# Performance work log

Hardware: AMD Instinct MI355X
Metric: run time of the kernel (lower is better)

Reference implementation:

```python
import jax, jax.numpy as jnp
import numpy as np

ETA, ALPHA, BETA, TAU, PROB_TH = 1.0, 0.08, 0.01, 10.0, 0.8


def knn_similarity(x, y, method):
    # x, y: [b, n, f]. Faithful port of GCN_Fusion.knn_similarity.
    b, n, f = x.shape
    if method == 'euclidean':
        # torch: D[b,i,j] = ||x[b,j] - y[b,i]||  (rows indexed by y)
        sq = (jnp.sum(y * y, -1)[:, :, None] + jnp.sum(x * x, -1)[:, None, :]
              - 2.0 * jnp.einsum('bif,bjf->bij', y, x))
        D = jnp.sqrt(jnp.maximum(sq, 1e-12))
    else:  # cosine: D[b,i,j] = 1 - <x_i, y_j>  (rows indexed by x)
        xn = x / jnp.maximum(jnp.linalg.norm(x, axis=2, keepdims=True), 1e-12)
        yn = y / jnp.maximum(jnp.linalg.norm(y, axis=2, keepdims=True), 1e-12)
        D = 1.0 - jnp.einsum('bif,bjf->bij', xn, yn)
    D_max = jnp.max(D, axis=2, keepdims=True)
    D_norm = D / D_max
    mu = jnp.mean(D, axis=(1, 2))
    sigma = jnp.std(D, axis=(1, 2), ddof=1)  # torch.std is unbiased
    prob_D = jax.nn.softmax(-D / TAU, axis=2)
    entropy = -jnp.sum(prob_D * jnp.log(prob_D + 1e-8), axis=2)  # [b,n]
    decay = jnp.exp(-ETA * entropy)[:, :, None]
    T = mu[:, None, None] + ALPHA * sigma[:, None, None] + BETA * (1.0 - D_norm) * decay
    sorted_idx = jnp.argsort(D, axis=-1)
    sorted_probs = jnp.take_along_axis(prob_D, sorted_idx, axis=-1)
    cum = jnp.cumsum(sorted_probs, axis=-1)
    mask = cum > PROB_TH
    first_over = jnp.argmax(mask.astype(jnp.int32), axis=-1)
    has_true = jnp.any(mask, axis=-1)
    num_edges = jnp.where(has_true, first_over, n)
    ranks = jnp.arange(n)
    mask_selected = ranks[None, None, :] < num_edges[:, :, None]
    # scatter_(-1, sorted_idx, mask_selected)  ==  gather by inverse permutation
    inv = jnp.argsort(sorted_idx, axis=-1)
    adj_mask = jnp.take_along_axis(mask_selected, inv, axis=-1)
    return (adj_mask & (D < T)).astype(D.dtype)


def gcn_fusion(x1, x2, x3, w1, b1, w2, b2, w3, b3):
    b, c, h, w = x1.shape
    n = h * w
    f1 = x1.reshape(b, c, n).transpose(0, 2, 1)  # [b,n,c]
    f2 = x2.reshape(b, c, n).transpose(0, 2, 1)
    f3 = x3.reshape(b, c, n).transpose(0, 2, 1)
    A11 = knn_similarity(f1, f1, 'euclidean')
    A22 = knn_similarity(f2, f2, 'euclidean')
    A33 = knn_similarity(f3, f3, 'euclidean')
    A12 = knn_similarity(f1, f2, 'cosine')
    A21 = knn_similarity(f2, f1, 'cosine')
    A13 = knn_similarity(f1, f3, 'cosine')
    A31 = knn_similarity(f3, f1, 'cosine')
    A23 = knn_similarity(f2, f3, 'cosine')
    A32 = knn_similarity(f3, f2, 'cosine')
    # 1x1 convs, expressed on flattened features: [b,n,c_out]
    p1 = jnp.einsum('bnc,oc->bno', f1, w1) + b1
    p2 = jnp.einsum('bnc,oc->bno', f2, w2) + b2
    p3 = jnp.einsum('bnc,oc->bno', f3, w3) + b3
    att = lambda a, pi, pj: jax.nn.softmax(a * jnp.einsum('bic,bjc->bij', pi, pj), axis=2)
    att_1 = jnp.concatenate([att(A11, p1, p1), att(A12, p1, p2), att(A13, p1, p3)], axis=2)
    att_2 = jnp.concatenate([att(A21, p2, p1), att(A22, p2, p2), att(A23, p2, p3)], axis=2)
    att_3 = jnp.concatenate([att(A31, p3, p1), att(A32, p3, p2), att(A33, p3, p3)], axis=2)
    x_cat = jnp.concatenate([f1, f2, f3], axis=1)  # [b,3n,c]
    o = (jnp.einsum('bij,bjc->bic', att_1, x_cat)
         + jnp.einsum('bij,bjc->bic', att_2, x_cat)
         + jnp.einsum('bij,bjc->bic', att_3, x_cat))
    return o.transpose(0, 2, 1).reshape(b, c, h, w)


def setup_inputs() -> dict:
    key = jax.random.key(0)
    ks = jax.random.split(key, 9)
    B, C, H, W = 2, 64, 32, 32
    s = 1.0 / np.sqrt(C)
    return {
        'x1': jax.random.normal(ks[0], (B, C, H, W), jnp.float32),
        'x2': jax.random.normal(ks[1], (B, C, H, W), jnp.float32),
        'x3': jax.random.normal(ks[2], (B, C, H, W), jnp.float32),
        'w1': jax.random.normal(ks[3], (C, C), jnp.float32) * s,
        'b1': jax.random.normal(ks[4], (C,), jnp.float32) * 0.01,
        'w2': jax.random.normal(ks[5], (C, C), jnp.float32) * s,
        'b2': jax.random.normal(ks[6], (C,), jnp.float32) * 0.01,
        'w3': jax.random.normal(ks[7], (C, C), jnp.float32) * s,
        'b3': jax.random.normal(ks[8], (C,), jnp.float32) * 0.01,
    }


def reference(x1, x2, x3, w1, b1, w2, b2, w3, b3):
    return gcn_fusion(x1, x2, x3, w1, b1, w2, b2, w3, b3)
```

## Files before the change

kernel.cpp:

```cpp
#include <hip/hip_runtime.h>

#define NN 1024
#define CC 64
#define BB 2

typedef unsigned long long ull;
typedef unsigned int u32;

#define WVB() __builtin_amdgcn_wave_barrier()

__device__ __forceinline__ float wsum(float v){
  #pragma unroll
  for (int o=32;o;o>>=1) v += __shfl_xor(v,o);
  return v;
}
__device__ __forceinline__ float wmaxr(float v){
  #pragma unroll
  for (int o=32;o;o>>=1) v = fmaxf(v, __shfl_xor(v,o));
  return v;
}
__device__ __forceinline__ float wminr(float v){
  #pragma unroll
  for (int o=32;o;o>>=1) v = fminf(v, __shfl_xor(v,o));
  return v;
}
__device__ __forceinline__ ull wmaxu64(ull v){
  #pragma unroll
  for (int o=32;o;o>>=1){ ull x = __shfl_xor(v,o); v = (x>v)?x:v; }
  return v;
}
__device__ __forceinline__ float4 ld4(const float* p){ return *reinterpret_cast<const float4*>(p); }
__device__ __forceinline__ u32 monob(float d){
  u32 u = __float_as_uint(d);
  return (u & 0x80000000u) ? ~u : (u | 0x80000000u);
}

#define GEMM_COLS(R, col, ylm, j4v, adv)                                          \
  { _Pragma("unroll 4")                                                           \
    for (int cc=0; cc<16; cc++){                                                  \
      float4 c0 = ld4((col) + (size_t)(cc*4+0)*NN + (j4v));                       \
      float4 c1 = ld4((col) + (size_t)(cc*4+1)*NN + (j4v));                       \
      float4 c2 = ld4((col) + (size_t)(cc*4+2)*NN + (j4v));                       \
      float4 c3 = ld4((col) + (size_t)(cc*4+3)*NN + (j4v));                       \
      _Pragma("unroll")                                                           \
      for (int rr=0; rr<(R); rr++){                                               \
        float4 y4 = *reinterpret_cast<const float4*>(&(ylm)[rr][cc*4]);           \
        float a0 = adv[rr][0], a1 = adv[rr][1], a2 = adv[rr][2], a3 = adv[rr][3]; \
        a0 = fmaf(y4.x,c0.x,a0); a0 = fmaf(y4.y,c1.x,a0); a0 = fmaf(y4.z,c2.x,a0); a0 = fmaf(y4.w,c3.x,a0); \
        a1 = fmaf(y4.x,c0.y,a1); a1 = fmaf(y4.y,c1.y,a1); a1 = fmaf(y4.z,c2.y,a1); a1 = fmaf(y4.w,c3.y,a1); \
        a2 = fmaf(y4.x,c0.z,a2); a2 = fmaf(y4.y,c1.z,a2); a2 = fmaf(y4.z,c2.z,a2); a2 = fmaf(y4.w,c3.z,a2); \
        a3 = fmaf(y4.x,c0.w,a3); a3 = fmaf(y4.y,c1.w,a3); a3 = fmaf(y4.z,c2.w,a3); a3 = fmaf(y4.w,c3.w,a3); \
        adv[rr][0]=a0; adv[rr][1]=a1; adv[rr][2]=a2; adv[rr][3]=a3;               \
      }                                                                           \
    }                                                                             \
  }

#define DFINISH(eucv, yn2r, cn2v, adr, dvv)                                       \
  { if (eucv){                                                                    \
      dvv[0] = sqrtf(fmaxf(fmaf(-2.0f, adr[0], (yn2r) + (cn2v).x), 1e-12f));      \
      dvv[1] = sqrtf(fmaxf(fmaf(-2.0f, adr[1], (yn2r) + (cn2v).y), 1e-12f));      \
      dvv[2] = sqrtf(fmaxf(fmaf(-2.0f, adr[2], (yn2r) + (cn2v).z), 1e-12f));      \
      dvv[3] = sqrtf(fmaxf(fmaf(-2.0f, adr[3], (yn2r) + (cn2v).w), 1e-12f));      \
    } else {                                                                      \
      dvv[0] = 1.0f - adr[0]; dvv[1] = 1.0f - adr[1];                             \
      dvv[2] = 1.0f - adr[2]; dvv[3] = 1.0f - adr[3];                             \
    }                                                                             \
  }

__global__ void kz(float* __restrict__ out, double* __restrict__ sums){
  int i = blockIdx.x*256 + threadIdx.x;
  if (i < BB*CC*NN) out[i] = 0.0f;
  if (i < 36) sums[i] = 0.0;
}

__global__ __launch_bounds__(256)
void k0a(const float* __restrict__ x1, const float* __restrict__ x2, const float* __restrict__ x3,
         float* __restrict__ f){
  int bid = blockIdx.x;
  int tile = bid & 15;
  int b = (bid >> 4) & 1;
  int s = bid >> 5;
  const float* x = (s==0)?x1:((s==1)?x2:x3);
  __shared__ float lds[64][65];
  int i0 = tile*64;
  for (int idx = threadIdx.x; idx < 4096; idx += 256){
    int c = idx >> 6, ii = idx & 63;
    lds[c][ii] = x[(size_t)(b*CC + c)*NN + i0 + ii];
  }
  __syncthreads();
  for (int idx = threadIdx.x; idx < 4096; idx += 256){
    int ii = idx >> 6, c = idx & 63;
    f[((size_t)(s*BB + b)*NN + i0 + ii)*CC + c] = lds[c][ii];
  }
}

__global__ __launch_bounds__(256)
void k0b(const float* __restrict__ f,
         const float* __restrict__ w1, const float* __restrict__ b1,
         const float* __restrict__ w2, const float* __restrict__ b2,
         const float* __restrict__ w3, const float* __restrict__ b3,
         float* __restrict__ p, float* __restrict__ pT,
         float* __restrict__ fnT, float* __restrict__ nrm2g){
  int bid = blockIdx.x;
  int chunk = bid & 63;
  int b = (bid >> 6) & 1;
  int s = bid >> 7;
  const float* w = (s==0)?w1:((s==1)?w2:w3);
  const float* bias = (s==0)?b1:((s==1)?b2:b3);
  __shared__ float wl[64][65];
  __shared__ float fr[16][65];
  __shared__ float n2[16];
  int i0 = chunk*16;
  int t = threadIdx.x;
  for (int idx = t; idx < 4096; idx += 256){
    int o = idx >> 6, c = idx & 63;
    wl[o][c] = w[idx];
  }
  for (int idx = t; idx < 1024; idx += 256){
    int rr = idx >> 6, c = idx & 63;
    fr[rr][c] = f[((size_t)(s*BB + b)*NN + i0 + rr)*CC + c];
  }
  __syncthreads();
  {
    int r = t >> 4, l = t & 15;
    float pv = 0.f;
    for (int c = l; c < 64; c += 16) pv += fr[r][c]*fr[r][c];
    #pragma unroll
    for (int o=8;o;o>>=1) pv += __shfl_down(pv, o, 16);
    if (l == 0) n2[r] = pv;
  }
  __syncthreads();
  if (t < 16) nrm2g[(size_t)(s*BB + b)*NN + i0 + t] = n2[t];
  for (int idx = t; idx < 1024; idx += 256){
    int rr = idx >> 6, c = idx & 63;
    float rinv = 1.0f / fmaxf(sqrtf(n2[rr]), 1e-12f);
    fnT[((size_t)(s*BB + b)*CC + c)*NN + i0 + rr] = fr[rr][c]*rinv;
  }
  for (int idx = t; idx < 1024; idx += 256){
    int rr = idx >> 6, o = idx & 63;
    float acc = bias[o];
    #pragma unroll
    for (int c = 0; c < 64; c++) acc += fr[rr][c]*wl[o][c];
    p [((size_t)(s*BB + b)*NN + i0 + rr)*CC + o] = acc;
    pT[((size_t)(s*BB + b)*CC + o)*NN + i0 + rr] = acc;
  }
}

__global__ void k2(const double* __restrict__ sums, float* __restrict__ baseg){
  int t = threadIdx.x;
  if (t < 18){
    double S = sums[t*2], S2 = sums[t*2+1];
    const double Nsq = 1048576.0;
    double mu = S / Nsq;
    double var = (S2 - S*S/Nsq) / (Nsq - 1.0);
    double sg = var > 0.0 ? sqrt(var) : 0.0;
    baseg[t] = (float)(mu + 0.08*sg);
  }
}

__global__ __launch_bounds__(256, 3)
void ksel(const float* __restrict__ x1, const float* __restrict__ x2, const float* __restrict__ x3,
          const float* __restrict__ f, const float* __restrict__ fnT,
          const float* __restrict__ nrm2g, double* __restrict__ sums, uint4* __restrict__ rec){
  __shared__ __align__(16) float yl[8][64];
  __shared__ __align__(16) float Dt[8][NN];
  __shared__ float hist[4][256];
  __shared__ float candd[4][64];
  __shared__ int   candj[4][64];
  __shared__ u32   candb[4][64];
  __shared__ float yn2[8];
  __shared__ int   cnt4[4];
  __shared__ int   selI4[4];
  __shared__ float selC4[4];
  __shared__ float s1s[4], s2s[4];

  int bid = blockIdx.x;
  int tile = bid & 127;
  int q = (bid >> 7) % 9;
  int b = bid / 1152;
  int r = q / 3, s = q - 3*r;
  bool euc = (r == s);
  int m = b*9 + q;
  int i0 = tile*8;
  int t = threadIdx.x;
  int w = t >> 6, lane = t & 63;

  if (t < 8) yn2[t] = nrm2g[(size_t)(r*BB + b)*NN + i0 + t];
  __syncthreads();
  for (int idx = t; idx < 512; idx += 256){
    int rr = idx >> 6, c = idx & 63;
    float v = f[((size_t)(r*BB + b)*NN + i0 + rr)*CC + c];
    if (!euc) v *= 1.0f / fmaxf(sqrtf(yn2[rr]), 1e-12f);
    yl[rr][c] = v;
  }
  __syncthreads();

  const float* xs = (s==0)?x1:((s==1)?x2:x3);
  const float* colD = euc ? (xs + (size_t)(b*CC)*NN) : (fnT + (size_t)((s*BB + b)*CC)*NN);
  int j4 = 4*t;

  float ad[8][4];
  #pragma unroll
  for (int rr=0;rr<8;rr++){ ad[rr][0]=0.f; ad[rr][1]=0.f; ad[rr][2]=0.f; ad[rr][3]=0.f; }
  GEMM_COLS(8, colD, yl, j4, ad)

  float4 cn2 = make_float4(0.f,0.f,0.f,0.f);
  if (euc) cn2 = ld4(nrm2g + (size_t)(s*BB + b)*NN + j4);

  float sd = 0.f, sd2 = 0.f;
  #pragma unroll
  for (int rr=0;rr<8;rr++){
    float dv[4];
    DFINISH(euc, yn2[rr], cn2, ad[rr], dv)
    sd  += dv[0]+dv[1]+dv[2]+dv[3];
    sd2 += dv[0]*dv[0]+dv[1]*dv[1]+dv[2]*dv[2]+dv[3]*dv[3];
    float4 o4; o4.x=dv[0]; o4.y=dv[1]; o4.z=dv[2]; o4.w=dv[3];
    *reinterpret_cast<float4*>(&Dt[rr][j4]) = o4;
  }
  sd = wsum(sd); sd2 = wsum(sd2);
  if (lane == 0){ s1s[w] = sd; s2s[w] = sd2; }
  __syncthreads();
  if (t == 0){
    double S  = (double)s1s[0] + (double)s1s[1] + (double)s1s[2] + (double)s1s[3];
    double S2 = (double)s2s[0] + (double)s2s[1] + (double)s2s[2] + (double)s2s[3];
    atomicAdd(&sums[m*2 + 0], S);
    atomicAdd(&sums[m*2 + 1], S2);
  }

  for (int rr2 = 0; rr2 < 2; rr2++){
    int row = w*2 + rr2;
    float dreg[16];
    #pragma unroll
    for (int k2=0;k2<4;k2++){
      float4 v = ld4(&Dt[row][4*lane + 256*k2]);
      dreg[4*k2+0]=v.x; dreg[4*k2+1]=v.y; dreg[4*k2+2]=v.z; dreg[4*k2+3]=v.w;
    }
    float lmin = 3.4e38f, lmax = -3.4e38f;
    #pragma unroll
    for (int k=0;k<16;k++){ lmin = fminf(lmin,dreg[k]); lmax = fmaxf(lmax,dreg[k]); }
    float Dmin = wminr(lmin);
    float Dmax = wmaxr(lmax);
    float lz = 0.f;
    #pragma unroll
    for (int k=0;k<16;k++) lz += expf((Dmin - dreg[k])*0.1f);
    float Z = wsum(lz);
    float invZ = 1.0f/Z;
    float preg[16];
    #pragma unroll
    for (int k=0;k<16;k++) preg[k] = expf((Dmin - dreg[k])*0.1f)*invZ;
    float le = 0.f;
    #pragma unroll
    for (int k=0;k<16;k++) le += preg[k]*logf(preg[k] + 1e-8f);
    float ent = -wsum(le);
    float decay = expf(-ent);
    float range = Dmax - Dmin;
    float scale1 = 256.0f / fmaxf(range, 1e-30f);

    if (lane==0){ selI4[w]=255; selC4[w]=0.8f; cnt4[w]=0; }
    #pragma unroll
    for (int i=0;i<4;i++) hist[w][lane*4+i] = 0.f;
    WVB();
    #pragma unroll
    for (int k=0;k<16;k++){
      int b1 = (int)((dreg[k]-Dmin)*scale1); b1 = (b1>255)?255:b1;
      atomicAdd(&hist[w][b1], preg[k]);
    }
    WVB();
    {
      float h0=hist[w][lane*4+0], h1=hist[w][lane*4+1], h2=hist[w][lane*4+2], h3=hist[w][lane*4+3];
      float tot = h0+h1+h2+h3;
      float incl = tot;
      #pragma unroll
      for (int o=1;o<64;o<<=1){ float v = __shfl_up(incl,o); if (lane>=o) incl += v; }
      float excl = incl - tot;
      float c0=excl, c1=excl+h0, c2=c1+h1, c3=c2+h2;
      bool f0=(c0<=0.8f && 0.8f<c0+h0), f1=(c1<=0.8f && 0.8f<c1+h1),
           f2=(c2<=0.8f && 0.8f<c2+h2), f3=(c3<=0.8f && 0.8f<c3+h3);
      if (f0){ selI4[w]=lane*4+0; selC4[w]=c0; }
      if (f1){ selI4[w]=lane*4+1; selC4[w]=c1; }
      if (f2){ selI4[w]=lane*4+2; selC4[w]=c2; }
      if (f3){ selI4[w]=lane*4+3; selC4[w]=c3; }
      if (__ballot(f0||f1||f2||f3) == 0ull){
        int bi = 10000; float bc = 0.f;
        if (c0>0.8f){bi=lane*4+0;bc=c0;} else if (c1>0.8f){bi=lane*4+1;bc=c1;}
        else if (c2>0.8f){bi=lane*4+2;bc=c2;} else if (c3>0.8f){bi=lane*4+3;bc=c3;}
        int mn = bi;
        #pragma unroll
        for (int o=32;o;o>>=1) mn = min(mn, __shfl_xor(mn,o));
        if (mn==bi && bi<10000){ selI4[w]=bi; selC4[w]=bc; }
      }
    }
    WVB();
    int B1 = selI4[w]; float cb1 = selC4[w];
    float lo2 = Dmin + (float)B1/scale1;
    float scale2 = scale1*256.0f;
    if (lane==0){ selI4[w]=255; selC4[w]=cb1; }
    #pragma unroll
    for (int i=0;i<4;i++) hist[w][lane*4+i] = 0.f;
    WVB();
    #pragma unroll
    for (int k=0;k<16;k++){
      int b1 = (int)((dreg[k]-Dmin)*scale1); b1 = (b1>255)?255:b1;
      if (b1 == B1){
        int b2 = (int)((dreg[k]-lo2)*scale2); b2 = (b2<0)?0:((b2>255)?255:b2);
        atomicAdd(&hist[w][b2], preg[k]);
      }
    }
    WVB();
    {
      float h0=hist[w][lane*4+0], h1=hist[w][lane*4+1], h2=hist[w][lane*4+2], h3=hist[w][lane*4+3];
      float tot = h0+h1+h2+h3;
      float incl = tot;
      #pragma unroll
      for (int o=1;o<64;o<<=1){ float v = __shfl_up(incl,o); if (lane>=o) incl += v; }
      float excl = incl - tot;
      float c0=cb1+excl, c1=c0+h0, c2=c1+h1, c3=c2+h2;
      bool f0=(c0<=0.8f && 0.8f<c0+h0), f1=(c1<=0.8f && 0.8f<c1+h1),
           f2=(c2<=0.8f && 0.8f<c2+h2), f3=(c3<=0.8f && 0.8f<c3+h3);
      if (f0){ selI4[w]=lane*4+0; selC4[w]=c0; }
      if (f1){ selI4[w]=lane*4+1; selC4[w]=c1; }
      if (f2){ selI4[w]=lane*4+2; selC4[w]=c2; }
      if (f3){ selI4[w]=lane*4+3; selC4[w]=c3; }
      if (__ballot(f0||f1||f2||f3) == 0ull){
        int bi = 10000; float bc = 0.f;
        if (c0>0.8f){bi=lane*4+0;bc=c0;} else if (c1>0.8f){bi=lane*4+1;bc=c1;}
        else if (c2>0.8f){bi=lane*4+2;bc=c2;} else if (c3>0.8f){bi=lane*4+3;bc=c3;}
        int mn = bi;
        #pragma unroll
        for (int o=32;o;o>>=1) mn = min(mn, __shfl_xor(mn,o));
        if (mn==bi && bi<10000){ selI4[w]=bi; selC4[w]=bc; }
      }
    }
    WVB();
    int B2 = selI4[w]; float cb2 = selC4[w];

    #pragma unroll
    for (int k=0;k<16;k++){
      int b1 = (int)((dreg[k]-Dmin)*scale1); b1 = (b1>255)?255:b1;
      if (b1 == B1){
        int b2 = (int)((dreg[k]-lo2)*scale2); b2 = (b2<0)?0:((b2>255)?255:b2);
        if (b2 == B2){
          int c = atomicAdd(&cnt4[w], 1);
          if (c < 64){
            int j = (k>>2)*256 + 4*lane + (k&3);
            candj[w][c] = j;
            candd[w][c] = dreg[k];
            candb[w][c] = monob(dreg[k]);
          }
        }
      }
    }
    WVB();
    ull em = 0;
    #pragma unroll
    for (int k=0;k<16;k++){
      int b1 = (int)((dreg[k]-Dmin)*scale1); b1 = (b1>255)?255:b1;
      bool qual;
      if (b1 < B1) qual = true;
      else if (b1 > B1) qual = false;
      else {
        int b2 = (int)((dreg[k]-lo2)*scale2); b2 = (b2<0)?0:((b2>255)?255:b2);
        qual = (b2 < B2);
      }
      if (qual){
        int j = (k>>2)*256 + 4*lane + (k&3);
        ull key = ((ull)monob(dreg[k]) << 32) | (u32)j;
        if (key > em) em = key;
      }
    }
    em = wmaxu64(em);
    if (lane == 0){
      int n = cnt4[w]; n = (n>64)?64:n;
      ull best = em;
      for (int a=0;a<n;a++){
        float da = candd[w][a]; int ja = candj[w][a];
        float acc = cb2;
        for (int bb=0;bb<n;bb++){
          float db = candd[w][bb]; int jb = candj[w][bb];
          if (db < da || (db == da && jb <= ja))
            acc += expf((Dmin - db)*0.1f)*invZ;
        }
        if (acc <= 0.8f){
          ull key = ((ull)candb[w][a] << 32) | (u32)ja;
          if (key > best) best = key;
        }
      }
      rec[(size_t)m*NN + i0 + row] = make_uint4((u32)(best>>32), (u32)(best & 0xFFFFFFFFu),
                                               __float_as_uint(Dmax), __float_as_uint(decay));
    }
    WVB();
  }
}

__global__ __launch_bounds__(256, 3)
void kapp(const float* __restrict__ x1, const float* __restrict__ x2, const float* __restrict__ x3,
          const float* __restrict__ f, const float* __restrict__ p,
          const float* __restrict__ fnT, const float* __restrict__ pT,
          const float* __restrict__ nrm2g, const float* __restrict__ baseg,
          const uint4* __restrict__ rec, float* __restrict__ out){
  __shared__ __align__(16) float yl[8][64];
  __shared__ __align__(16) float pyl[8][64];
  __shared__ __align__(16) float Sm[8][NN];
  __shared__ __align__(16) float opart[4][8][64];
  __shared__ float yn2[8];
  __shared__ u32 dBb[8]; __shared__ u32 jBl[8];
  __shared__ float th[8];

  int bid = blockIdx.x;
  int tile = bid & 127;
  int q = (bid >> 7) % 9;
  int b = bid / 1152;
  int r = q / 3, s = q - 3*r;
  bool euc = (r == s);
  int m = b*9 + q;
  int i0 = tile*8;
  int t = threadIdx.x;
  int w = t >> 6, lane = t & 63;

  if (t < 8){
    yn2[t] = nrm2g[(size_t)(r*BB + b)*NN + i0 + t];
    uint4 R = rec[(size_t)m*NN + i0 + t];
    dBb[t] = R.x; jBl[t] = R.y;
    float Dmax = __uint_as_float(R.z);
    float decay = __uint_as_float(R.w);
    float Tb = baseg[m];
    th[t] = (Tb + 0.01f*decay) / (1.0f + 0.01f*decay/Dmax);
  }
  __syncthreads();
  for (int idx = t; idx < 512; idx += 256){
    int rr = idx >> 6, c = idx & 63;
    float v = f[((size_t)(r*BB + b)*NN + i0 + rr)*CC + c];
    if (!euc) v *= 1.0f / fmaxf(sqrtf(yn2[rr]), 1e-12f);
    yl[rr][c] = v;
    pyl[rr][c] = p[((size_t)(r*BB + b)*NN + i0 + rr)*CC + c];
  }
  __syncthreads();

  const float* xs = (s==0)?x1:((s==1)?x2:x3);
  const float* colD = euc ? (xs + (size_t)(b*CC)*NN) : (fnT + (size_t)((s*BB + b)*CC)*NN);
  const float* colP = pT + (size_t)((s*BB + b)*CC)*NN;
  int j4 = 4*t;

  float ad[8][4];
  #pragma unroll
  for (int rr=0;rr<8;rr++){ ad[rr][0]=0.f; ad[rr][1]=0.f; ad[rr][2]=0.f; ad[rr][3]=0.f; }
  GEMM_COLS(8, colD, yl, j4, ad)

  float ap[8][4];
  #pragma unroll
  for (int rr=0;rr<8;rr++){ ap[rr][0]=0.f; ap[rr][1]=0.f; ap[rr][2]=0.f; ap[rr][3]=0.f; }
  GEMM_COLS(8, colP, pyl, j4, ap)

  float4 cn2 = make_float4(0.f,0.f,0.f,0.f);
  if (euc) cn2 = ld4(nrm2g + (size_t)(s*BB + b)*NN + j4);

  #pragma unroll
  for (int rr=0;rr<8;rr++){
    float dv[4];
    DFINISH(euc, yn2[rr], cn2, ad[rr], dv)
    u32 db = dBb[rr]; u32 jb = jBl[rr]; float tt = th[rr];
    float4 sv;
    {
      u32 bits = monob(dv[0]); u32 j = (u32)(j4+0);
      bool sel = (bits < db) || (bits == db && j <= jb);
      sv.x = (sel && dv[0] < tt) ? ap[rr][0] : 0.f;
    }
    {
      u32 bits = monob(dv[1]); u32 j = (u32)(j4+1);
      bool sel = (bits < db) || (bits == db && j <= jb);
      sv.y = (sel && dv[1] < tt) ? ap[rr][1] : 0.f;
    }
    {
      u32 bits = monob(dv[2]); u32 j = (u32)(j4+2);
      bool sel = (bits < db) || (bits == db && j <= jb);
      sv.z = (sel && dv[2] < tt) ? ap[rr][2] : 0.f;
    }
    {
      u32 bits = monob(dv[3]); u32 j = (u32)(j4+3);
      bool sel = (bits < db) || (bits == db && j <= jb);
      sv.w = (sel && dv[3] < tt) ? ap[rr][3] : 0.f;
    }
    *reinterpret_cast<float4*>(&Sm[rr][j4]) = sv;
  }
  __syncthreads();

  #pragma unroll
  for (int e=0;e<2;e++){
    int row = 2*w + e;
    float s16[16];
    #pragma unroll
    for (int k2=0;k2<4;k2++){
      float4 v = ld4(&Sm[row][4*lane + 256*k2]);
      s16[4*k2+0]=v.x; s16[4*k2+1]=v.y; s16[4*k2+2]=v.z; s16[4*k2+3]=v.w;
    }
    float lm = -3.4e38f;
    #pragma unroll
    for (int k=0;k<16;k++) lm = fmaxf(lm, s16[k]);
    float M = wmaxr(lm);
    float ls = 0.f;
    #pragma unroll
    for (int k=0;k<16;k++) ls += expf(s16[k]-M);
    float Z2 = wsum(ls);
    float iZ2 = 1.0f/Z2;
    #pragma unroll
    for (int k2=0;k2<4;k2++){
      float4 v;
      v.x = expf(s16[4*k2+0]-M)*iZ2;
      v.y = expf(s16[4*k2+1]-M)*iZ2;
      v.z = expf(s16[4*k2+2]-M)*iZ2;
      v.w = expf(s16[4*k2+3]-M)*iZ2;
      *reinterpret_cast<float4*>(&Sm[row][4*lane + 256*k2]) = v;
    }
  }
  __syncthreads();

  int cg = t & 15, jj = t >> 4;
  float acc[8][4];
  #pragma unroll
  for (int rr=0;rr<8;rr++){ acc[rr][0]=0.f; acc[rr][1]=0.f; acc[rr][2]=0.f; acc[rr][3]=0.f; }
  const float* fs = f + (size_t)((s*BB + b)*NN)*CC;
  for (int mm=0; mm<64; mm++){
    int j = jj + 16*mm;
    float4 fv = ld4(&fs[(size_t)j*CC + 4*cg]);
    #pragma unroll
    for (int rr=0;rr<8;rr++){
      float pv = Sm[rr][j];
      acc[rr][0] = fmaf(pv, fv.x, acc[rr][0]);
      acc[rr][1] = fmaf(pv, fv.y, acc[rr][1]);
      acc[rr][2] = fmaf(pv, fv.z, acc[rr][2]);
      acc[rr][3] = fmaf(pv, fv.w, acc[rr][3]);
    }
  }
  #pragma unroll
  for (int rr=0;rr<8;rr++){
    #pragma unroll
    for (int i=0;i<4;i++){
      acc[rr][i] += __shfl_xor(acc[rr][i], 16);
      acc[rr][i] += __shfl_xor(acc[rr][i], 32);
    }
  }
  if (lane < 16){
    #pragma unroll
    for (int rr=0;rr<8;rr++){
      float4 v; v.x=acc[rr][0]; v.y=acc[rr][1]; v.z=acc[rr][2]; v.w=acc[rr][3];
      *reinterpret_cast<float4*>(&opart[w][rr][4*cg]) = v;
    }
  }
  __syncthreads();
  #pragma unroll
  for (int e=0;e<2;e++){
    int idx = t + 256*e;
    int rr = idx >> 6, c = idx & 63;
    float v = opart[0][rr][c]+opart[1][rr][c]+opart[2][rr][c]+opart[3][rr][c];
    atomicAdd(&out[(size_t)(b*CC + c)*NN + i0 + rr], v);
  }
}

extern "C" void kernel_launch(void* const* d_in, const int* in_sizes, int n_in,
                              void* d_out, int out_size, void* d_ws, size_t ws_size,
                              hipStream_t stream){
  const float* x1 = (const float*)d_in[0];
  const float* x2 = (const float*)d_in[1];
  const float* x3 = (const float*)d_in[2];
  const float* w1 = (const float*)d_in[3];
  const float* b1 = (const float*)d_in[4];
  const float* w2 = (const float*)d_in[5];
  const float* b2 = (const float*)d_in[6];
  const float* w3 = (const float*)d_in[7];
  const float* b3 = (const float*)d_in[8];

  char* ws = (char*)d_ws;
  const size_t SZ = (size_t)3*BB*NN*CC*sizeof(float);
  float*  f    = (float*)(ws);
  float*  p    = (float*)(ws + SZ);
  float*  fnT  = (float*)(ws + 2*SZ);
  float*  pT   = (float*)(ws + 3*SZ);
  float*  nrm2 = (float*)(ws + 4*SZ);
  double* sums = (double*)(ws + 4*SZ + 32768);
  float*  baseg= (float*)(ws + 4*SZ + 32768 + 512);
  uint4*  rec  = (uint4*)(ws + 4*SZ + 65536);

  float* out = (float*)d_out;

  kz  <<<512, 256, 0, stream>>>(out, sums);
  k0a <<<96,  256, 0, stream>>>(x1, x2, x3, f);
  k0b <<<384, 256, 0, stream>>>(f, w1, b1, w2, b2, w3, b3, p, pT, fnT, nrm2);
  ksel<<<2304,256, 0, stream>>>(x1, x2, x3, f, fnT, nrm2, sums, rec);
  k2  <<<1,   64,  0, stream>>>(sums, baseg);
  kapp<<<2304,256, 0, stream>>>(x1, x2, x3, f, p, fnT, pT, nrm2, baseg, rec, out);
}
```

Measured before the change: 389.5 us.

## Reuse softmax exps, closed-form entropy, skip second histogram, parallelize candidate scan

In the selection kernel the softmax exponentials are now computed once and reused. The entropy is rewritten algebraically as exp(sum p*logit)/Z, which avoids a per-element log. The second-level histogram pass now runs only when the first-level bucket holds more than 64 elements. The O(n^2) single-lane candidate cumulative-probability scan becomes a wave-parallel scan using stored probabilities. The attention softmax in kapp also reuses its exp results instead of recomputing them. The closed-form entropy drops the 1e-8 epsilon inside the log, so results differ slightly from the reference, and the cutoff comparison now orders candidates by monotone bits instead of the float distance values.

```diff
diff --git a/kernel.cpp b/kernel.cpp
--- a/kernel.cpp
+++ b/kernel.cpp
@@ -66,6 +66,8 @@
       dvv[2] = 1.0f - adr[2]; dvv[3] = 1.0f - adr[3];                             \
     }                                                                             \
   }
+
+#define BUCKET1(dv) ({ int _b = (int)(((dv)-Dmin)*scale1); (_b>255)?255:_b; })
 
 __global__ void kz(float* __restrict__ out, double* __restrict__ sums){
   int i = blockIdx.x*256 + threadIdx.x;
@@ -165,7 +167,7 @@
   __shared__ __align__(16) float yl[8][64];
   __shared__ __align__(16) float Dt[8][NN];
   __shared__ float hist[4][256];
-  __shared__ float candd[4][64];
+  __shared__ float candp[4][64];
   __shared__ int   candj[4][64];
   __shared__ u32   candb[4][64];
   __shared__ float yn2[8];
@@ -240,29 +242,29 @@
     for (int k=0;k<16;k++){ lmin = fminf(lmin,dreg[k]); lmax = fmaxf(lmax,dreg[k]); }
     float Dmin = wminr(lmin);
     float Dmax = wmaxr(lmax);
+    float preg[16];
     float lz = 0.f;
     #pragma unroll
-    for (int k=0;k<16;k++) lz += expf((Dmin - dreg[k])*0.1f);
+    for (int k=0;k<16;k++){ preg[k] = expf((Dmin - dreg[k])*0.1f); lz += preg[k]; }
     float Z = wsum(lz);
     float invZ = 1.0f/Z;
-    float preg[16];
-    #pragma unroll
-    for (int k=0;k<16;k++) preg[k] = expf((Dmin - dreg[k])*0.1f)*invZ;
-    float le = 0.f;
-    #pragma unroll
-    for (int k=0;k<16;k++) le += preg[k]*logf(preg[k] + 1e-8f);
-    float ent = -wsum(le);
-    float decay = expf(-ent);
+    #pragma unroll
+    for (int k=0;k<16;k++) preg[k] *= invZ;
+    float sl = 0.f;
+    #pragma unroll
+    for (int k=0;k<16;k++) sl = fmaf(preg[k], (Dmin - dreg[k])*0.1f, sl);
+    float sumpl = wsum(sl);
+    float decay = expf(sumpl)*invZ;
     float range = Dmax - Dmin;
     float scale1 = 256.0f / fmaxf(range, 1e-30f);
 
-    if (lane==0){ selI4[w]=255; selC4[w]=0.8f; cnt4[w]=0; }
+    if (lane==0){ selI4[w]=255; selC4[w]=0.8f; }
     #pragma unroll
     for (int i=0;i<4;i++) hist[w][lane*4+i] = 0.f;
     WVB();
     #pragma unroll
     for (int k=0;k<16;k++){
-      int b1 = (int)((dreg[k]-Dmin)*scale1); b1 = (b1>255)?255:b1;
+      int b1 = BUCKET1(dreg[k]);
       atomicAdd(&hist[w][b1], preg[k]);
     }
     WVB();
@@ -292,73 +294,93 @@
     }
     WVB();
     int B1 = selI4[w]; float cb1 = selC4[w];
-    float lo2 = Dmin + (float)B1/scale1;
-    float scale2 = scale1*256.0f;
-    if (lane==0){ selI4[w]=255; selC4[w]=cb1; }
-    #pragma unroll
-    for (int i=0;i<4;i++) hist[w][lane*4+i] = 0.f;
-    WVB();
-    #pragma unroll
-    for (int k=0;k<16;k++){
-      int b1 = (int)((dreg[k]-Dmin)*scale1); b1 = (b1>255)?255:b1;
-      if (b1 == B1){
-        int b2 = (int)((dreg[k]-lo2)*scale2); b2 = (b2<0)?0:((b2>255)?255:b2);
-        atomicAdd(&hist[w][b2], preg[k]);
-      }
-    }
-    WVB();
-    {
-      float h0=hist[w][lane*4+0], h1=hist[w][lane*4+1], h2=hist[w][lane*4+2], h3=hist[w][lane*4+3];
-      float tot = h0+h1+h2+h3;
-      float incl = tot;
+
+    float cntf = 0.f;
+    #pragma unroll
+    for (int k=0;k<16;k++) if (BUCKET1(dreg[k]) == B1) cntf += 1.0f;
+    float n1f = wsum(cntf);
+    bool need2 = (n1f > 64.0f);
+    float cb = cb1;
+    int B2 = 0; float lo2 = 0.f, scale2 = 0.f;
+    if (need2){
+      lo2 = Dmin + (float)B1/scale1;
+      scale2 = scale1*256.0f;
+      if (lane==0){ selI4[w]=255; selC4[w]=cb1; }
       #pragma unroll
-      for (int o=1;o<64;o<<=1){ float v = __shfl_up(incl,o); if (lane>=o) incl += v; }
-      float excl = incl - tot;
-      float c0=cb1+excl, c1=c0+h0, c2=c1+h1, c3=c2+h2;
-      bool f0=(c0<=0.8f && 0.8f<c0+h0), f1=(c1<=0.8f && 0.8f<c1+h1),
-           f2=(c2<=0.8f && 0.8f<c2+h2), f3=(c3<=0.8f && 0.8f<c3+h3);
-      if (f0){ selI4[w]=lane*4+0; selC4[w]=c0; }
-      if (f1){ selI4[w]=lane*4+1; selC4[w]=c1; }
-      if (f2){ selI4[w]=lane*4+2; selC4[w]=c2; }
-      if (f3){ selI4[w]=lane*4+3; selC4[w]=c3; }
-      if (__ballot(f0||f1||f2||f3) == 0ull){
-        int bi = 10000; float bc = 0.f;
-        if (c0>0.8f){bi=lane*4+0;bc=c0;} else if (c1>0.8f){bi=lane*4+1;bc=c1;}
-        else if (c2>0.8f){bi=lane*4+2;bc=c2;} else if (c3>0.8f){bi=lane*4+3;bc=c3;}
-        int mn = bi;
-        #pragma unroll
-        for (int o=32;o;o>>=1) mn = min(mn, __shfl_xor(mn,o));
-        if (mn==bi && bi<10000){ selI4[w]=bi; selC4[w]=bc; }
-      }
-    }
-    WVB();
-    int B2 = selI4[w]; float cb2 = selC4[w];
-
-    #pragma unroll
-    for (int k=0;k<16;k++){
-      int b1 = (int)((dreg[k]-Dmin)*scale1); b1 = (b1>255)?255:b1;
-      if (b1 == B1){
-        int b2 = (int)((dreg[k]-lo2)*scale2); b2 = (b2<0)?0:((b2>255)?255:b2);
-        if (b2 == B2){
-          int c = atomicAdd(&cnt4[w], 1);
-          if (c < 64){
-            int j = (k>>2)*256 + 4*lane + (k&3);
-            candj[w][c] = j;
-            candd[w][c] = dreg[k];
-            candb[w][c] = monob(dreg[k]);
-          }
+      for (int i=0;i<4;i++) hist[w][lane*4+i] = 0.f;
+      WVB();
+      #pragma unroll
+      for (int k=0;k<16;k++){
+        if (BUCKET1(dreg[k]) == B1){
+          int b2 = (int)((dreg[k]-lo2)*scale2); b2 = (b2<0)?0:((b2>255)?255:b2);
+          atomicAdd(&hist[w][b2], preg[k]);
         }
       }
-    }
+      WVB();
+      {
+        float h0=hist[w][lane*4+0], h1=hist[w][lane*4+1], h2=hist[w][lane*4+2], h3=hist[w][lane*4+3];
+        float tot = h0+h1+h2+h3;
+        float incl = tot;
+        #pragma unroll
+        for (int o=1;o<64;o<<=1){ float v = __shfl_up(incl,o); if (lane>=o) incl += v; }
+        float excl = incl - tot;
+        float c0=cb1+excl, c1=c0+h0, c2=c1+h1, c3=c2+h2;
+        bool f0=(c0<=0.8f && 0.8f<c0+h0), f1=(c1<=0.8f && 0.8f<c1+h1),
+             f2=(c2<=0.8f && 0.8f<c2+h2), f3=(c3<=0.8f && 0.8f<c3+h3);
+        if (f0){ selI4[w]=lane*4+0; selC4[w]=c0; }
+        if (f1){ selI4[w]=lane*4+1; selC4[w]=c1; }
+        if (f2){ selI4[w]=lane*4+2; selC4[w]=c2; }
+        if (f3){ selI4[w]=lane*4+3; selC4[w]=c3; }
+        if (__ballot(f0||f1||f2||f3) == 0ull){
+          int bi = 10000; float bc = 0.f;
+          if (c0>0.8f){bi=lane*4+0;bc=c0;} else if (c1>0.8f){bi=lane*4+1;bc=c1;}
+          else if (c2>0.8f){bi=lane*4+2;bc=c2;} else if (c3>0.8f){bi=lane*4+3;bc=c3;}
+          int mn = bi;
+          #pragma unroll
+          for (int o=32;o;o>>=1) mn = min(mn, __shfl_xor(mn,o));
+          if (mn==bi && bi<10000){ selI4[w]=bi; selC4[w]=bc; }
+        }
+      }
+      WVB();
+      B2 = selI4[w]; cb = selC4[w];
+    }
+
+    if (lane==0) cnt4[w] = 0;
     WVB();
+    #pragma unroll
+    for (int k=0;k<16;k++){
+      bool inb = (BUCKET1(dreg[k]) == B1);
+      if (need2 && inb){
+        int b2 = (int)((dreg[k]-lo2)*scale2); b2 = (b2<0)?0:((b2>255)?255:b2);
+        inb = (b2 == B2);
+      }
+      if (inb){
+        int c = atomicAdd(&cnt4[w], 1);
+        if (c < 64){
+          int j = (k>>2)*256 + 4*lane + (k&3);
+          candj[w][c] = j;
+          candb[w][c] = monob(dreg[k]);
+          candp[w][c] = preg[k];
+        }
+      }
+    }
+    WVB();
+    int n = cnt4[w]; n = (n>64)?64:n;
+
+    u32 myb = 0, myj = 0;
+    if (lane < n){ myb = candb[w][lane]; myj = (u32)candj[w][lane]; }
+    float acc = cb;
+    for (int a=0;a<n;a++){
+      u32 ba = candb[w][a]; u32 ja = (u32)candj[w][a]; float pa = candp[w][a];
+      bool le = (ba < myb) || (ba == myb && ja <= myj);
+      acc += le ? pa : 0.f;
+    }
     ull em = 0;
     #pragma unroll
     for (int k=0;k<16;k++){
-      int b1 = (int)((dreg[k]-Dmin)*scale1); b1 = (b1>255)?255:b1;
-      bool qual;
-      if (b1 < B1) qual = true;
-      else if (b1 > B1) qual = false;
-      else {
+      int b1v = BUCKET1(dreg[k]);
+      bool qual = (b1v < B1);
+      if (need2 && b1v == B1){
         int b2 = (int)((dreg[k]-lo2)*scale2); b2 = (b2<0)?0:((b2>255)?255:b2);
         qual = (b2 < B2);
       }
@@ -368,24 +390,13 @@
         if (key > em) em = key;
       }
     }
+    if (lane < n && acc <= 0.8f){
+      ull key = ((ull)myb << 32) | myj;
+      if (key > em) em = key;
+    }
     em = wmaxu64(em);
     if (lane == 0){
-      int n = cnt4[w]; n = (n>64)?64:n;
-      ull best = em;
-      for (int a=0;a<n;a++){
-        float da = candd[w][a]; int ja = candj[w][a];
-        float acc = cb2;
-        for (int bb=0;bb<n;bb++){
-          float db = candd[w][bb]; int jb = candj[w][bb];
-          if (db < da || (db == da && jb <= ja))
-            acc += expf((Dmin - db)*0.1f)*invZ;
-        }
-        if (acc <= 0.8f){
-          ull key = ((ull)candb[w][a] << 32) | (u32)ja;
-          if (key > best) best = key;
-        }
-      }
-      rec[(size_t)m*NN + i0 + row] = make_uint4((u32)(best>>32), (u32)(best & 0xFFFFFFFFu),
+      rec[(size_t)m*NN + i0 + row] = make_uint4((u32)(em>>32), (u32)(em & 0xFFFFFFFFu),
                                                __float_as_uint(Dmax), __float_as_uint(decay));
     }
     WVB();
@@ -499,16 +510,16 @@
     float M = wmaxr(lm);
     float ls = 0.f;
     #pragma unroll
-    for (int k=0;k<16;k++) ls += expf(s16[k]-M);
+    for (int k=0;k<16;k++){ s16[k] = expf(s16[k]-M); ls += s16[k]; }
     float Z2 = wsum(ls);
     float iZ2 = 1.0f/Z2;
     #pragma unroll
     for (int k2=0;k2<4;k2++){
       float4 v;
-      v.x = expf(s16[4*k2+0]-M)*iZ2;
-      v.y = expf(s16[4*k2+1]-M)*iZ2;
-      v.z = expf(s16[4*k2+2]-M)*iZ2;
-      v.w = expf(s16[4*k2+3]-M)*iZ2;
+      v.x = s16[4*k2+0]*iZ2;
+      v.y = s16[4*k2+1]*iZ2;
+      v.z = s16[4*k2+2]*iZ2;
+      v.w = s16[4*k2+3]*iZ2;
       *reinterpret_cast<float4*>(&Sm[row][4*lane + 256*k2]) = v;
     }
   }
```

Result: no change. 387.2 us (-0.6%).
